# Performance work log

Hardware: AMD Instinct MI355X
Metric: run time of the kernel (lower is better)

Reference implementation:

```python
import jax, jax.numpy as jnp
import numpy as np

SHRINK_THRES = 0.0025
R_THRES = 1.0
EPS = 1e-12


def setup_inputs() -> dict:
    key = jax.random.key(0)
    k1, k2 = jax.random.split(key)
    N, L, D = 16384, 4096, 1024  # samples, memory slots (lan_dim), fea_dim
    x = jax.random.normal(k1, (N, D), dtype=jnp.float32)
    stdv = 1.0 / np.sqrt(D)
    weight = jax.random.uniform(k2, (L, D), dtype=jnp.float32, minval=-stdv, maxval=stdv)
    return {"x": x, "weight": weight}


def reference(x, weight):
    # memory addressing: att = softmax(x @ W^T)  -> [N, L]
    att = jax.nn.softmax(x @ weight.T, axis=1)
    # hard_shrink_relu: relu(a - lambd) * a / (|a - lambd| + eps)
    shifted = att - SHRINK_THRES
    att = jax.nn.relu(shifted) * att / (jnp.abs(shifted) + EPS)
    # L1 normalize along dim 1 (F.normalize p=1, eps=1e-12)
    l1 = jnp.sum(jnp.abs(att), axis=1, keepdims=True)
    att = att / jnp.maximum(l1, EPS)
    # reconstruct from memory: [N, D]
    output = att @ weight
    # nearest landmark per sample (detached gather in original)
    ind = jnp.argmax(att, axis=1)                      # [N]
    nl = weight[ind]                                   # [N, D]
    # second-nearest: overwrite argmax slot with the row minimum, re-argmax
    rows = jnp.arange(att.shape[0])
    row_min = jnp.min(att, axis=1)
    att2 = att.at[rows, ind].set(row_min)
    ind2 = jnp.argmax(att2, axis=1)
    nl2 = weight[ind2]                                 # [N, D]
    # centroid-distance filter (original returns list of indices; we return a
    # jit-compatible boolean mask over samples instead)
    cen = jnp.mean(weight, axis=0)                     # [D]
    dist = jnp.sqrt(jnp.sum((x - cen) ** 2, axis=1))   # [N]
    col_mask = dist < R_THRES                          # [N] bool
    return (output, att, nl, nl2, col_mask)
```

## Files before the change

kernel.cpp:

```cpp
#include <hip/hip_runtime.h>
#include <cmath>

#define NS 16384
#define LS 4096
#define DF 1024
#define SHRINK_T 0.0025f
#define EPS_T 1e-12f

using f16 = _Float16;
using f16x4 = __attribute__((ext_vector_type(4))) _Float16;
using f16x8 = __attribute__((ext_vector_type(8))) _Float16;
using f32x16 = __attribute__((ext_vector_type(16))) float;

#define NSEG 64

__global__ void split_kernel(const float* __restrict__ src,
                             f16* __restrict__ hi, f16* __restrict__ lo, int n4) {
    int i = blockIdx.x * 256 + threadIdx.x;
    if (i >= n4) return;
    float4 v = reinterpret_cast<const float4*>(src)[i];
    f16x4 h, l;
    h[0] = (f16)v.x; h[1] = (f16)v.y; h[2] = (f16)v.z; h[3] = (f16)v.w;
    l[0] = (f16)(v.x - (float)h[0]);
    l[1] = (f16)(v.y - (float)h[1]);
    l[2] = (f16)(v.z - (float)h[2]);
    l[3] = (f16)(v.w - (float)h[3]);
    reinterpret_cast<f16x4*>(hi)[i] = h;
    reinterpret_cast<f16x4*>(lo)[i] = l;
}

__global__ void centroid_part_kernel(const float* __restrict__ w, float* __restrict__ part) {
    const int c = blockIdx.x * 256 + threadIdx.x;
    const int seg = blockIdx.y;
    const int l0 = seg * (LS / NSEG);
    float acc = 0.f;
    for (int l = 0; l < LS / NSEG; ++l)
        acc += w[(size_t)(l0 + l) * DF + c];
    part[(size_t)seg * DF + c] = acc;
}

__global__ void centroid_sum_kernel(const float* __restrict__ part, float* __restrict__ cen) {
    const int c = blockIdx.x * 256 + threadIdx.x;
    float acc = 0.f;
    for (int s = 0; s < NSEG; ++s) acc += part[(size_t)s * DF + c];
    cen[c] = acc * (1.0f / (float)LS);
}

#define BM 128
#define BN 128
#define BK 32

#define GLOAD16(gptr, lptr)                                                    \
    __builtin_amdgcn_global_load_lds(                                          \
        (const __attribute__((address_space(1))) void*)(gptr),                 \
        (__attribute__((address_space(3))) void*)(lptr), 16, 0, 0)

__device__ __forceinline__ int swz_s(int r) { return (r & 3) ^ ((r >> 2) & 1); }

__global__ __launch_bounds__(256) void gemm_f16_kernel(
    const f16* __restrict__ xh, const f16* __restrict__ xl,
    const f16* __restrict__ wh, const f16* __restrict__ wl,
    float* __restrict__ S, int r0, int rowsChunk)
{
    __shared__ __align__(16) f16 Ah[BM * BK];
    __shared__ __align__(16) f16 Al[BM * BK];
    __shared__ __align__(16) f16 Bh[BN * BK];
    __shared__ __align__(16) f16 Bl[BN * BK];

    const int t = threadIdx.x;
    const int lane = t & 63;
    const int wv = t >> 6;
    const int wr = (wv >> 1) * 64;
    const int wc = (wv & 1) * 64;
    const int rowBase = r0 + blockIdx.y * BM;
    const int colBase = blockIdx.x * BN;

    f32x16 acc[2][2];
#pragma unroll
    for (int m = 0; m < 2; ++m)
#pragma unroll
        for (int n = 0; n < 2; ++n)
#pragma unroll
            for (int j = 0; j < 16; ++j) acc[m][n][j] = 0.f;

    const int c32 = lane & 31;
    const int kh = lane >> 5;

    const int sr_lo = t >> 2;
    const int cc_lo = ((t & 3) ^ swz_s(sr_lo)) * 8;
    const int sr_hi = 64 + sr_lo;
    const int cc_hi = ((t & 3) ^ swz_s(sr_hi)) * 8;
    int ga_lo = rowBase + sr_lo; if (ga_lo >= NS) ga_lo = NS - 1;
    int ga_hi = rowBase + sr_hi; if (ga_hi >= NS) ga_hi = NS - 1;
    const size_t aoff_lo = (size_t)ga_lo * DF + cc_lo;
    const size_t aoff_hi = (size_t)ga_hi * DF + cc_hi;
    const size_t boff_lo = (size_t)(colBase + sr_lo) * DF + cc_lo;
    const size_t boff_hi = (size_t)(colBase + sr_hi) * DF + cc_hi;
    const int lb_lo = (wv * 16) * BK;
    const int lb_hi = (64 + wv * 16) * BK;

#define STAGE(k0)                                        \
    do {                                                 \
        GLOAD16(xh + aoff_lo + (k0), &Ah[lb_lo]);        \
        GLOAD16(xl + aoff_lo + (k0), &Al[lb_lo]);        \
        GLOAD16(wh + boff_lo + (k0), &Bh[lb_lo]);        \
        GLOAD16(wl + boff_lo + (k0), &Bl[lb_lo]);        \
        GLOAD16(xh + aoff_hi + (k0), &Ah[lb_hi]);        \
        GLOAD16(xl + aoff_hi + (k0), &Al[lb_hi]);        \
        GLOAD16(wh + boff_hi + (k0), &Bh[lb_hi]);        \
        GLOAD16(wl + boff_hi + (k0), &Bl[lb_hi]);        \
    } while (0)

    STAGE(0);

    constexpr int NKT = DF / BK;
    for (int kt = 0; kt < NKT; ++kt) {
        __syncthreads();

        f16x8 amh[2][2], aml[2][2], bnh[2][2], bnl[2][2];
#pragma unroll
        for (int s = 0; s < 2; ++s) {
#pragma unroll
            for (int m = 0; m < 2; ++m) {
                const int r = wr + m * 32 + c32;
                const int q = ((s * 2 + kh) ^ swz_s(r)) * 8;
                amh[s][m] = *(const f16x8*)&Ah[r * BK + q];
                aml[s][m] = *(const f16x8*)&Al[r * BK + q];
            }
#pragma unroll
            for (int n = 0; n < 2; ++n) {
                const int c = wc + n * 32 + c32;
                const int q = ((s * 2 + kh) ^ swz_s(c)) * 8;
                bnh[s][n] = *(const f16x8*)&Bh[c * BK + q];
                bnl[s][n] = *(const f16x8*)&Bl[c * BK + q];
            }
        }

        __syncthreads();

        if (kt + 1 < NKT) STAGE((kt + 1) * BK);

#pragma unroll
        for (int s = 0; s < 2; ++s)
#pragma unroll
            for (int m = 0; m < 2; ++m)
#pragma unroll
                for (int n = 0; n < 2; ++n) {
                    acc[m][n] = __builtin_amdgcn_mfma_f32_32x32x16_f16(amh[s][m], bnh[s][n], acc[m][n], 0, 0, 0);
                    acc[m][n] = __builtin_amdgcn_mfma_f32_32x32x16_f16(amh[s][m], bnl[s][n], acc[m][n], 0, 0, 0);
                    acc[m][n] = __builtin_amdgcn_mfma_f32_32x32x16_f16(aml[s][m], bnh[s][n], acc[m][n], 0, 0, 0);
                }
    }
#undef STAGE

#pragma unroll
    for (int m = 0; m < 2; ++m) {
        const int rb = blockIdx.y * BM + wr + m * 32 + 4 * kh;
#pragma unroll
        for (int n = 0; n < 2; ++n) {
            const int cc = colBase + wc + n * 32 + c32;
#pragma unroll
            for (int reg = 0; reg < 16; ++reg) {
                const int rr = rb + (reg & 3) + 8 * (reg >> 2);
                if (rr < rowsChunk)
                    S[(size_t)rr * LS + cc] = acc[m][n][reg];
            }
        }
    }
}

__global__ __launch_bounds__(256) void pass2_kernel(
    const float* __restrict__ S, const float* __restrict__ x,
    const float* __restrict__ w, const float* __restrict__ cen,
    float* __restrict__ out, int r0)
{
    constexpr int T = 256;
    __shared__ __align__(16) float att_lds[LS];
    __shared__ float red[T];
    __shared__ int redi[T];

    const int t = threadIdx.x;
    const size_t row = (size_t)r0 + blockIdx.x;
    const float4* s4 = (const float4*)(S + (size_t)blockIdx.x * (size_t)LS);

    float* const out_output = out;
    float* const out_att  = out + (size_t)NS * DF;
    float* const out_nl   = out + (size_t)NS * DF + (size_t)NS * LS;
    float* const out_nl2  = out + (size_t)2 * NS * DF + (size_t)NS * LS;
    float* const out_mask = out + (size_t)3 * NS * DF + (size_t)NS * LS;

    float sv[16];
    float mx = -INFINITY;
#pragma unroll
    for (int i = 0; i < 4; ++i) {
        float4 v = s4[i * 256 + t];
        sv[i * 4 + 0] = v.x; sv[i * 4 + 1] = v.y;
        sv[i * 4 + 2] = v.z; sv[i * 4 + 3] = v.w;
        mx = fmaxf(mx, fmaxf(fmaxf(v.x, v.y), fmaxf(v.z, v.w)));
    }
    red[t] = mx;
    __syncthreads();
    for (int off = 128; off >= 1; off >>= 1) {
        if (t < off) red[t] = fmaxf(red[t], red[t + off]);
        __syncthreads();
    }
    const float m = red[0];
    __syncthreads();

    float zs = 0.f;
#pragma unroll
    for (int i = 0; i < 16; ++i) {
        sv[i] = expf(sv[i] - m);
        zs += sv[i];
    }
    red[t] = zs;
    __syncthreads();
    for (int off = 128; off >= 1; off >>= 1) {
        if (t < off) red[t] += red[t + off];
        __syncthreads();
    }
    const float Z = red[0];
    __syncthreads();

    float l1 = 0.f;
#pragma unroll
    for (int i = 0; i < 16; ++i) {
        float a = sv[i] / Z;
        float r = a - SHRINK_T;
        float v = (r > 0.f) ? (r * a) / (r + EPS_T) : 0.f;
        sv[i] = v;
        l1 += v;
    }
    red[t] = l1;
    __syncthreads();
    for (int off = 128; off >= 1; off >>= 1) {
        if (t < off) red[t] += red[t + off];
        __syncthreads();
    }
    const float nrm = fmaxf(red[0], EPS_T);
    __syncthreads();

    float bv = -INFINITY; int bi = LS;
    float mn = INFINITY;
    float4* const attl4 = (float4*)att_lds;
    float4* const att4o = (float4*)(out_att + row * LS);
#pragma unroll
    for (int i = 0; i < 4; ++i) {
        float4 vn4;
        vn4.x = sv[i * 4 + 0] / nrm; vn4.y = sv[i * 4 + 1] / nrm;
        vn4.z = sv[i * 4 + 2] / nrm; vn4.w = sv[i * 4 + 3] / nrm;
        sv[i * 4 + 0] = vn4.x; sv[i * 4 + 1] = vn4.y;
        sv[i * 4 + 2] = vn4.z; sv[i * 4 + 3] = vn4.w;
        attl4[i * 256 + t] = vn4;
        att4o[i * 256 + t] = vn4;
#pragma unroll
        for (int c = 0; c < 4; ++c) {
            const float v = sv[i * 4 + c];
            const int j = i * 1024 + 4 * t + c;
            if (v > bv) { bv = v; bi = j; }
            mn = fminf(mn, v);
        }
    }
    __syncthreads();

    red[t] = bv; redi[t] = bi;
    __syncthreads();
    for (int off = 128; off >= 1; off >>= 1) {
        if (t < off) {
            float ov = red[t + off]; int oi = redi[t + off];
            if (ov > red[t] || (ov == red[t] && oi < redi[t])) { red[t] = ov; redi[t] = oi; }
        }
        __syncthreads();
    }
    const int ind = redi[0];
    __syncthreads();

    red[t] = mn;
    __syncthreads();
    for (int off = 128; off >= 1; off >>= 1) {
        if (t < off) red[t] = fminf(red[t], red[t + off]);
        __syncthreads();
    }
    const float rowmin = red[0];
    __syncthreads();

    bv = -INFINITY; bi = LS;
#pragma unroll
    for (int i = 0; i < 4; ++i)
#pragma unroll
        for (int c = 0; c < 4; ++c) {
            const int j = i * 1024 + 4 * t + c;
            const float vv = (j == ind) ? rowmin : sv[i * 4 + c];
            if (vv > bv) { bv = vv; bi = j; }
        }
    red[t] = bv; redi[t] = bi;
    __syncthreads();
    for (int off = 128; off >= 1; off >>= 1) {
        if (t < off) {
            float ov = red[t + off]; int oi = redi[t + off];
            if (ov > red[t] || (ov == red[t] && oi < redi[t])) { red[t] = ov; redi[t] = oi; }
        }
        __syncthreads();
    }
    const int ind2 = redi[0];
    __syncthreads();

    const int lane = t & 63;
    float4 oa = {0.f, 0.f, 0.f, 0.f};
    for (int k0 = 0; k0 < LS; k0 += 64) {
        float av = att_lds[k0 + lane];
        unsigned long long msk = __ballot(av > 0.f);
        while (msk) {
            int b = __ffsll((unsigned long long)msk) - 1;
            msk &= msk - 1;
            float vv = att_lds[k0 + b];
            float4 wv4 = ((const float4*)(w + (size_t)(k0 + b) * DF))[t];
            oa.x = fmaf(vv, wv4.x, oa.x);
            oa.y = fmaf(vv, wv4.y, oa.y);
            oa.z = fmaf(vv, wv4.z, oa.z);
            oa.w = fmaf(vv, wv4.w, oa.w);
        }
    }
    ((float4*)(out_output + row * DF))[t] = oa;

    ((float4*)(out_nl  + row * DF))[t] = ((const float4*)(w + (size_t)ind  * DF))[t];
    ((float4*)(out_nl2 + row * DF))[t] = ((const float4*)(w + (size_t)ind2 * DF))[t];

    float4 xv = ((const float4*)(x + row * DF))[t];
    float4 cv = ((const float4*)cen)[t];
    float ds = 0.f;
    ds = fmaf(xv.x - cv.x, xv.x - cv.x, ds);
    ds = fmaf(xv.y - cv.y, xv.y - cv.y, ds);
    ds = fmaf(xv.z - cv.z, xv.z - cv.z, ds);
    ds = fmaf(xv.w - cv.w, xv.w - cv.w, ds);
    red[t] = ds;
    __syncthreads();
    for (int off = 128; off >= 1; off >>= 1) {
        if (t < off) red[t] += red[t + off];
        __syncthreads();
    }
    if (t == 0) {
        float dist = sqrtf(red[0]);
        out_mask[row] = (dist < 1.0f) ? 1.0f : 0.0f;
    }
}

extern "C" void kernel_launch(void* const* d_in, const int* in_sizes, int n_in,
                              void* d_out, int out_size, void* d_ws, size_t ws_size,
                              hipStream_t stream)
{
    const float* x = (const float*)d_in[0];
    const float* w = (const float*)d_in[1];
    float* out = (float*)d_out;

    float* cen = (float*)d_ws;
    float* part = cen + DF;
    f16* xh = (f16*)(part + (size_t)NSEG * DF);
    f16* xl = xh + (size_t)NS * DF;
    f16* wh = xl + (size_t)NS * DF;
    f16* wl = wh + (size_t)LS * DF;
    float* S = (float*)(wl + (size_t)LS * DF);

    const size_t head_bytes = sizeof(float) * (DF + (size_t)NSEG * DF)
                            + (size_t)2 * 2 * NS * DF + (size_t)2 * 2 * LS * DF;
    long cap_rows = (long)((ws_size - head_bytes) / (sizeof(float) * LS));
    if (cap_rows > NS) cap_rows = NS;
    if (cap_rows < 1) cap_rows = 1;
    int chunk = (cap_rows >= BM) ? (int)(cap_rows - (cap_rows % BM)) : (int)cap_rows;

    centroid_part_kernel<<<dim3(DF / 256, NSEG), 256, 0, stream>>>(w, part);
    centroid_sum_kernel<<<DF / 256, 256, 0, stream>>>(part, cen);
    split_kernel<<<(NS * DF / 4 + 255) / 256, 256, 0, stream>>>(x, xh, xl, NS * DF / 4);
    split_kernel<<<(LS * DF / 4 + 255) / 256, 256, 0, stream>>>(w, wh, wl, LS * DF / 4);

    for (int r0 = 0; r0 < NS; r0 += chunk) {
        int rows = (NS - r0 < chunk) ? (NS - r0) : chunk;
        dim3 grid((LS + BN - 1) / BN, (rows + BM - 1) / BM);
        gemm_f16_kernel<<<grid, 256, 0, stream>>>(xh, xl, wh, wl, S, r0, rows);
        pass2_kernel<<<rows, 256, 0, stream>>>(S, x, w, cen, out, r0);
    }
}
```

Before: 590.9 us.

## Widen GEMM block tile to 128x256 and drop LDS swizzle

The split-f16 GEMM block tile grows from 128x128 to 128x256, so each wave now computes a 64x128 sub-tile. This is meant to improve operand reuse and cut global and LDS traffic per MFMA. The XOR swizzle on the LDS layout and the clamp on out-of-range rows are removed, which simplifies address arithmetic. In exchange the accumulator register footprint doubles, which can lower occupancy, and the unswizzled LDS reads may hit bank conflicts.

```diff
diff --git a/kernel.cpp b/kernel.cpp
--- a/kernel.cpp
+++ b/kernel.cpp
@@ -47,15 +47,14 @@
 }
 
 #define BM 128
-#define BN 128
+#define BN 256
 #define BK 32
+#define NKT (DF / BK)
 
 #define GLOAD16(gptr, lptr)                                                    \
     __builtin_amdgcn_global_load_lds(                                          \
         (const __attribute__((address_space(1))) void*)(gptr),                 \
         (__attribute__((address_space(3))) void*)(lptr), 16, 0, 0)
-
-__device__ __forceinline__ int swz_s(int r) { return (r & 3) ^ ((r >> 2) & 1); }
 
 __global__ __launch_bounds__(256) void gemm_f16_kernel(
     const f16* __restrict__ xh, const f16* __restrict__ xl,
@@ -70,74 +69,77 @@
     const int t = threadIdx.x;
     const int lane = t & 63;
     const int wv = t >> 6;
-    const int wr = (wv >> 1) * 64;
-    const int wc = (wv & 1) * 64;
+    const int wvm = wv >> 1;
+    const int wvn = wv & 1;
     const int rowBase = r0 + blockIdx.y * BM;
     const int colBase = blockIdx.x * BN;
 
-    f32x16 acc[2][2];
+    f32x16 acc[2][4];
 #pragma unroll
     for (int m = 0; m < 2; ++m)
 #pragma unroll
-        for (int n = 0; n < 2; ++n)
+        for (int n = 0; n < 4; ++n)
 #pragma unroll
             for (int j = 0; j < 16; ++j) acc[m][n][j] = 0.f;
 
     const int c32 = lane & 31;
     const int kh = lane >> 5;
 
-    const int sr_lo = t >> 2;
-    const int cc_lo = ((t & 3) ^ swz_s(sr_lo)) * 8;
-    const int sr_hi = 64 + sr_lo;
-    const int cc_hi = ((t & 3) ^ swz_s(sr_hi)) * 8;
-    int ga_lo = rowBase + sr_lo; if (ga_lo >= NS) ga_lo = NS - 1;
-    int ga_hi = rowBase + sr_hi; if (ga_hi >= NS) ga_hi = NS - 1;
-    const size_t aoff_lo = (size_t)ga_lo * DF + cc_lo;
-    const size_t aoff_hi = (size_t)ga_hi * DF + cc_hi;
-    const size_t boff_lo = (size_t)(colBase + sr_lo) * DF + cc_lo;
-    const size_t boff_hi = (size_t)(colBase + sr_hi) * DF + cc_hi;
-    const int lb_lo = (wv * 16) * BK;
-    const int lb_hi = (64 + wv * 16) * BK;
-
-#define STAGE(k0)                                        \
-    do {                                                 \
-        GLOAD16(xh + aoff_lo + (k0), &Ah[lb_lo]);        \
-        GLOAD16(xl + aoff_lo + (k0), &Al[lb_lo]);        \
-        GLOAD16(wh + boff_lo + (k0), &Bh[lb_lo]);        \
-        GLOAD16(wl + boff_lo + (k0), &Bl[lb_lo]);        \
-        GLOAD16(xh + aoff_hi + (k0), &Ah[lb_hi]);        \
-        GLOAD16(xl + aoff_hi + (k0), &Al[lb_hi]);        \
-        GLOAD16(wh + boff_hi + (k0), &Bh[lb_hi]);        \
-        GLOAD16(wl + boff_hi + (k0), &Bl[lb_hi]);        \
+    const int srow = t >> 2;
+    const int scol = (t & 3) * 8;
+    const size_t aoff0 = (size_t)(rowBase + srow) * DF + scol;
+    const size_t aoff1 = (size_t)(rowBase + 64 + srow) * DF + scol;
+    const size_t boff0 = (size_t)(colBase + srow) * DF + scol;
+    const size_t boff1 = (size_t)(colBase + 64 + srow) * DF + scol;
+    const size_t boff2 = (size_t)(colBase + 128 + srow) * DF + scol;
+    const size_t boff3 = (size_t)(colBase + 192 + srow) * DF + scol;
+    const int lb0 = wv * 512;
+    const int lb1 = wv * 512 + 2048;
+    const int lb2 = wv * 512 + 4096;
+    const int lb3 = wv * 512 + 6144;
+
+#define STAGE(k0)                                   \
+    do {                                            \
+        GLOAD16(xh + aoff0 + (k0), &Ah[lb0]);       \
+        GLOAD16(xh + aoff1 + (k0), &Ah[lb1]);       \
+        GLOAD16(xl + aoff0 + (k0), &Al[lb0]);       \
+        GLOAD16(xl + aoff1 + (k0), &Al[lb1]);       \
+        GLOAD16(wh + boff0 + (k0), &Bh[lb0]);       \
+        GLOAD16(wh + boff1 + (k0), &Bh[lb1]);       \
+        GLOAD16(wh + boff2 + (k0), &Bh[lb2]);       \
+        GLOAD16(wh + boff3 + (k0), &Bh[lb3]);       \
+        GLOAD16(wl + boff0 + (k0), &Bl[lb0]);       \
+        GLOAD16(wl + boff1 + (k0), &Bl[lb1]);       \
+        GLOAD16(wl + boff2 + (k0), &Bl[lb2]);       \
+        GLOAD16(wl + boff3 + (k0), &Bl[lb3]);       \
     } while (0)
 
+    const int baseA = (wvm * 64 + c32) * BK + kh * 8;
+    const int baseB = (wvn * 128 + c32) * BK + kh * 8;
+
     STAGE(0);
 
-    constexpr int NKT = DF / BK;
     for (int kt = 0; kt < NKT; ++kt) {
         __syncthreads();
 
-        f16x8 amh[2][2], aml[2][2], bnh[2][2], bnl[2][2];
+        f16x8 amh[2][2], aml[2][2], bnh[2][4], bnl[2][4];
 #pragma unroll
         for (int s = 0; s < 2; ++s) {
 #pragma unroll
             for (int m = 0; m < 2; ++m) {
-                const int r = wr + m * 32 + c32;
-                const int q = ((s * 2 + kh) ^ swz_s(r)) * 8;
-                amh[s][m] = *(const f16x8*)&Ah[r * BK + q];
-                aml[s][m] = *(const f16x8*)&Al[r * BK + q];
+                const int off = baseA + m * 32 * BK + s * 16;
+                amh[s][m] = *(const f16x8*)&Ah[off];
+                aml[s][m] = *(const f16x8*)&Al[off];
             }
 #pragma unroll
-            for (int n = 0; n < 2; ++n) {
-                const int c = wc + n * 32 + c32;
-                const int q = ((s * 2 + kh) ^ swz_s(c)) * 8;
-                bnh[s][n] = *(const f16x8*)&Bh[c * BK + q];
-                bnl[s][n] = *(const f16x8*)&Bl[c * BK + q];
+            for (int n = 0; n < 4; ++n) {
+                const int off = baseB + n * 32 * BK + s * 16;
+                bnh[s][n] = *(const f16x8*)&Bh[off];
+                bnl[s][n] = *(const f16x8*)&Bl[off];
             }
         }
 
         __syncthreads();
-
         if (kt + 1 < NKT) STAGE((kt + 1) * BK);
 
 #pragma unroll
@@ -145,7 +147,7 @@
 #pragma unroll
             for (int m = 0; m < 2; ++m)
 #pragma unroll
-                for (int n = 0; n < 2; ++n) {
+                for (int n = 0; n < 4; ++n) {
                     acc[m][n] = __builtin_amdgcn_mfma_f32_32x32x16_f16(amh[s][m], bnh[s][n], acc[m][n], 0, 0, 0);
                     acc[m][n] = __builtin_amdgcn_mfma_f32_32x32x16_f16(amh[s][m], bnl[s][n], acc[m][n], 0, 0, 0);
                     acc[m][n] = __builtin_amdgcn_mfma_f32_32x32x16_f16(aml[s][m], bnh[s][n], acc[m][n], 0, 0, 0);
@@ -155,10 +157,10 @@
 
 #pragma unroll
     for (int m = 0; m < 2; ++m) {
-        const int rb = blockIdx.y * BM + wr + m * 32 + 4 * kh;
-#pragma unroll
-        for (int n = 0; n < 2; ++n) {
-            const int cc = colBase + wc + n * 32 + c32;
+        const int rb = blockIdx.y * BM + wvm * 64 + m * 32 + 4 * kh;
+#pragma unroll
+        for (int n = 0; n < 4; ++n) {
+            const int cc = colBase + wvn * 128 + n * 32 + c32;
 #pragma unroll
             for (int reg = 0; reg < 16; ++reg) {
                 const int rr = rb + (reg & 3) + 8 * (reg >> 2);
```

Result: slower. 730.1 us (+23.6%).

## Double-buffer GEMM LDS tiles with two-stage prefetch and explicit waitcnt barriers

Applied to the files above, without the earlier changes.

The f16 split-precision GEMM now keeps two LDS buffers per operand and prefetches tile k+2 while computing tile k, using explicit s_waitcnt vmcnt and s_barrier instead of __syncthreads. The aim is to hide global-to-LDS load latency behind the MFMA work. The XOR swizzle on LDS rows is also removed, which simplifies addressing but may bring back LDS bank conflicts on the 16-byte reads. LDS use per block doubles, which can reduce occupancy.

```diff
diff --git a/kernel.cpp b/kernel.cpp
--- a/kernel.cpp
+++ b/kernel.cpp
@@ -49,23 +49,22 @@
 #define BM 128
 #define BN 128
 #define BK 32
+#define NKT (DF / BK)
 
 #define GLOAD16(gptr, lptr)                                                    \
     __builtin_amdgcn_global_load_lds(                                          \
         (const __attribute__((address_space(1))) void*)(gptr),                 \
         (__attribute__((address_space(3))) void*)(lptr), 16, 0, 0)
-
-__device__ __forceinline__ int swz_s(int r) { return (r & 3) ^ ((r >> 2) & 1); }
 
 __global__ __launch_bounds__(256) void gemm_f16_kernel(
     const f16* __restrict__ xh, const f16* __restrict__ xl,
     const f16* __restrict__ wh, const f16* __restrict__ wl,
     float* __restrict__ S, int r0, int rowsChunk)
 {
-    __shared__ __align__(16) f16 Ah[BM * BK];
-    __shared__ __align__(16) f16 Al[BM * BK];
-    __shared__ __align__(16) f16 Bh[BN * BK];
-    __shared__ __align__(16) f16 Bl[BN * BK];
+    __shared__ __align__(16) f16 Ah[2][BM * BK];
+    __shared__ __align__(16) f16 Al[2][BM * BK];
+    __shared__ __align__(16) f16 Bh[2][BN * BK];
+    __shared__ __align__(16) f16 Bl[2][BN * BK];
 
     const int t = threadIdx.x;
     const int lane = t & 63;
@@ -87,58 +86,63 @@
     const int kh = lane >> 5;
 
     const int sr_lo = t >> 2;
-    const int cc_lo = ((t & 3) ^ swz_s(sr_lo)) * 8;
+    const int cc = (t & 3) * 8;
     const int sr_hi = 64 + sr_lo;
-    const int cc_hi = ((t & 3) ^ swz_s(sr_hi)) * 8;
     int ga_lo = rowBase + sr_lo; if (ga_lo >= NS) ga_lo = NS - 1;
     int ga_hi = rowBase + sr_hi; if (ga_hi >= NS) ga_hi = NS - 1;
-    const size_t aoff_lo = (size_t)ga_lo * DF + cc_lo;
-    const size_t aoff_hi = (size_t)ga_hi * DF + cc_hi;
-    const size_t boff_lo = (size_t)(colBase + sr_lo) * DF + cc_lo;
-    const size_t boff_hi = (size_t)(colBase + sr_hi) * DF + cc_hi;
-    const int lb_lo = (wv * 16) * BK;
-    const int lb_hi = (64 + wv * 16) * BK;
-
-#define STAGE(k0)                                        \
-    do {                                                 \
-        GLOAD16(xh + aoff_lo + (k0), &Ah[lb_lo]);        \
-        GLOAD16(xl + aoff_lo + (k0), &Al[lb_lo]);        \
-        GLOAD16(wh + boff_lo + (k0), &Bh[lb_lo]);        \
-        GLOAD16(wl + boff_lo + (k0), &Bl[lb_lo]);        \
-        GLOAD16(xh + aoff_hi + (k0), &Ah[lb_hi]);        \
-        GLOAD16(xl + aoff_hi + (k0), &Al[lb_hi]);        \
-        GLOAD16(wh + boff_hi + (k0), &Bh[lb_hi]);        \
-        GLOAD16(wl + boff_hi + (k0), &Bl[lb_hi]);        \
+    const size_t aoff_lo = (size_t)ga_lo * DF + cc;
+    const size_t aoff_hi = (size_t)ga_hi * DF + cc;
+    const size_t boff_lo = (size_t)(colBase + sr_lo) * DF + cc;
+    const size_t boff_hi = (size_t)(colBase + sr_hi) * DF + cc;
+    const int lb_lo = wv * 512;
+    const int lb_hi = 2048 + wv * 512;
+
+#define STAGE(k0, b)                                      \
+    do {                                                  \
+        GLOAD16(xh + aoff_lo + (k0), &Ah[b][lb_lo]);      \
+        GLOAD16(xl + aoff_lo + (k0), &Al[b][lb_lo]);      \
+        GLOAD16(wh + boff_lo + (k0), &Bh[b][lb_lo]);      \
+        GLOAD16(wl + boff_lo + (k0), &Bl[b][lb_lo]);      \
+        GLOAD16(xh + aoff_hi + (k0), &Ah[b][lb_hi]);      \
+        GLOAD16(xl + aoff_hi + (k0), &Al[b][lb_hi]);      \
+        GLOAD16(wh + boff_hi + (k0), &Bh[b][lb_hi]);      \
+        GLOAD16(wl + boff_hi + (k0), &Bl[b][lb_hi]);      \
     } while (0)
 
-    STAGE(0);
-
-    constexpr int NKT = DF / BK;
+    const int baseA = (wr + c32) * BK + kh * 8;
+    const int baseB = (wc + c32) * BK + kh * 8;
+
+    STAGE(0, 0);
+    STAGE(BK, 1);
+
     for (int kt = 0; kt < NKT; ++kt) {
-        __syncthreads();
+        const int b = kt & 1;
+        if (kt == NKT - 1) asm volatile("s_waitcnt vmcnt(0)" ::: "memory");
+        else               asm volatile("s_waitcnt vmcnt(8)" ::: "memory");
+        __builtin_amdgcn_sched_barrier(0);
+        __builtin_amdgcn_s_barrier();
 
         f16x8 amh[2][2], aml[2][2], bnh[2][2], bnl[2][2];
 #pragma unroll
         for (int s = 0; s < 2; ++s) {
 #pragma unroll
             for (int m = 0; m < 2; ++m) {
-                const int r = wr + m * 32 + c32;
-                const int q = ((s * 2 + kh) ^ swz_s(r)) * 8;
-                amh[s][m] = *(const f16x8*)&Ah[r * BK + q];
-                aml[s][m] = *(const f16x8*)&Al[r * BK + q];
+                const int off = baseA + m * 32 * BK + s * 16;
+                amh[s][m] = *(const f16x8*)&Ah[b][off];
+                aml[s][m] = *(const f16x8*)&Al[b][off];
             }
 #pragma unroll
             for (int n = 0; n < 2; ++n) {
-                const int c = wc + n * 32 + c32;
-                const int q = ((s * 2 + kh) ^ swz_s(c)) * 8;
-                bnh[s][n] = *(const f16x8*)&Bh[c * BK + q];
-                bnl[s][n] = *(const f16x8*)&Bl[c * BK + q];
+                const int off = baseB + n * 32 * BK + s * 16;
+                bnh[s][n] = *(const f16x8*)&Bh[b][off];
+                bnl[s][n] = *(const f16x8*)&Bl[b][off];
             }
         }
-
-        __syncthreads();
-
-        if (kt + 1 < NKT) STAGE((kt + 1) * BK);
+        asm volatile("s_waitcnt lgkmcnt(0)" ::: "memory");
+        __builtin_amdgcn_sched_barrier(0);
+        __builtin_amdgcn_s_barrier();
+
+        if (kt + 2 < NKT) STAGE((kt + 2) * BK, b);
 
 #pragma unroll
         for (int s = 0; s < 2; ++s)
@@ -158,12 +162,12 @@
         const int rb = blockIdx.y * BM + wr + m * 32 + 4 * kh;
 #pragma unroll
         for (int n = 0; n < 2; ++n) {
-            const int cc = colBase + wc + n * 32 + c32;
+            const int cc2 = colBase + wc + n * 32 + c32;
 #pragma unroll
             for (int reg = 0; reg < 16; ++reg) {
                 const int rr = rb + (reg & 3) + 8 * (reg >> 2);
                 if (rr < rowsChunk)
-                    S[(size_t)rr * LS + cc] = acc[m][n][reg];
+                    S[(size_t)rr * LS + cc2] = acc[m][n][reg];
             }
         }
     }
```

Measured after the change: 618.7 us. 1.05x slower.
